# Kernel optimization log

Measured on AMD Instinct MI355X. Metric: run time of the kernel, lower is better.

## Reference

```python
import jax, jax.numpy as jnp
import numpy as np
from jax import lax

B, H, W, C = 4, 96, 96, 256
F = 256
KH = KW = 3
K = KH * KW
DG = 1
CG = C // DG
SH = SW = 1
DH = DW = 1
PAD_T = (DH * (KH - 1)) // 2  # 'same' padding (top/left) for 3x3 dil 1
PAD_L = (DW * (KW - 1)) // 2


def setup_inputs() -> dict:
    key = jax.random.key(0)
    k1, k2, k3 = jax.random.split(key, 3)
    x = jax.random.normal(k1, (B, H, W, C), jnp.float32)
    # offset/mask conv weights (orig init zeros; small random to exercise sampling)
    om_kernel = jax.random.normal(k2, (KH, KW, C, DG * 3 * K), jnp.float32) * 0.01
    om_bias = jnp.zeros((DG * 3 * K,), jnp.float32)
    stdv = 1.0 / np.sqrt(C * KH * KW)
    kernel = jax.random.uniform(k3, (K * C, F), jnp.float32, -stdv, stdv)
    bias = jnp.zeros((F,), jnp.float32)
    return {"x": x, "om_kernel": om_kernel, "om_bias": om_bias, "kernel": kernel, "bias": bias}


def reference(x, om_kernel, om_bias, kernel, bias):
    Bx, Hx, Wx, Cx = x.shape
    # offset/mask prediction conv (NHWC, 'SAME', matches keras Conv2D)
    om = lax.conv_general_dilated(
        x, om_kernel, (SH, SW), "SAME", rhs_dilation=(DH, DW),
        dimension_numbers=("NHWC", "HWIO", "NHWC")) + om_bias
    Ho, Wo = om.shape[1], om.shape[2]
    off = om[..., : 2 * DG * K].reshape(Bx, Ho, Wo, DG, K, 2)  # (dy, dx) per group/kpoint
    mask = jax.nn.sigmoid(om[..., 2 * DG * K :]).reshape(Bx, Ho, Wo, DG, K) * 2.0

    # base sampling grid: y = ho*SH - PAD_T + ki*DH (+ dy), similarly x
    base_y = (jnp.arange(Ho) * SH - PAD_T)[:, None] + (jnp.arange(KH) * DH)[None, :]  # [Ho,KH]
    base_x = (jnp.arange(Wo) * SW - PAD_L)[:, None] + (jnp.arange(KW) * DW)[None, :]  # [Wo,KW]
    gy = jnp.broadcast_to(base_y[:, None, :, None], (Ho, Wo, KH, KW)).reshape(Ho, Wo, K)
    gx = jnp.broadcast_to(base_x[None, :, None, :], (Ho, Wo, KH, KW)).reshape(Ho, Wo, K)

    py = gy[None, :, :, None, :].astype(x.dtype) + off[..., 0]  # [B,Ho,Wo,DG,K]
    px = gx[None, :, :, None, :].astype(x.dtype) + off[..., 1]

    # reorder to [B, N, DG] with N = Ho*Wo*K (K varies fastest after spatial)
    N = Ho * Wo * K
    py = py.transpose(0, 1, 2, 4, 3).reshape(Bx, N, DG)
    px = px.transpose(0, 1, 2, 4, 3).reshape(Bx, N, DG)
    mask_t = mask.transpose(0, 1, 2, 4, 3).reshape(Bx, N, DG)

    y0 = jnp.floor(py)
    x0 = jnp.floor(px)
    fy = py - y0
    fx = px - x0

    xf = x.reshape(Bx, Hx * Wx, DG, CG)
    val = jnp.zeros((Bx, N, DG, CG), x.dtype)
    for yi, wy in ((y0, 1.0 - fy), (y0 + 1.0, fy)):
        for xi, wx in ((x0, 1.0 - fx), (x0 + 1.0, fx)):
            valid = (yi >= 0) & (yi < Hx) & (xi >= 0) & (xi < Wx)
            yc = jnp.clip(yi, 0, Hx - 1).astype(jnp.int32)
            xc = jnp.clip(xi, 0, Wx - 1).astype(jnp.int32)
            lin = yc * Wx + xc  # [B,N,DG]
            g = jnp.take_along_axis(xf, lin[..., None], axis=1)  # [B,N,DG,CG]
            val = val + g * (wy * wx * valid.astype(x.dtype))[..., None]

    # modulate and im2col -> GEMM
    cols = (val * mask_t[..., None]).reshape(Bx, Ho * Wo, K * Cx)
    out = jnp.matmul(cols, kernel).reshape(Bx, Ho, Wo, -1) + bias
    return out
```

## Files before the change

kernel.cpp:

```cpp
#include <hip/hip_runtime.h>
#include <hip/hip_bf16.h>
#include <stdint.h>
#include <stddef.h>


namespace {
constexpr int H  = 96, W = 96, C = 256, F = 256;
constexpr int HP = 98;
constexpr int NP = 4 * 96 * 96;
constexpr int KC = 9 * 256;

constexpr int NB_PAD  = 4 * HP * HP / 8;
constexpr int NB_OMW  = 9 * 32;
constexpr int NB_WT   = (KC / 64) * (F / 64);
constexpr int NB_ZERO = NP * 32 * 4 / 4096;
}

typedef __attribute__((ext_vector_type(8))) short bf16x8;
typedef __attribute__((ext_vector_type(4))) float floatx4;

__device__ __forceinline__ void load_lds16(const void* g, void* l) {
  __builtin_amdgcn_global_load_lds((const __attribute__((address_space(1))) void*)g,
                                   (__attribute__((address_space(3))) void*)l,
                                   16, 0, 0);
}

__device__ __forceinline__ uint32_t pk2(float lo, float hi) {
  __hip_bfloat162 t = __float22bfloat162_rn(float2{lo, hi});
  return *reinterpret_cast<uint32_t*>(&t);
}

__device__ __forceinline__ void acc8(uint4 v, float w, float* a) {
  a[0] += w * __uint_as_float(v.x << 16); a[1] += w * __uint_as_float(v.x & 0xffff0000u);
  a[2] += w * __uint_as_float(v.y << 16); a[3] += w * __uint_as_float(v.y & 0xffff0000u);
  a[4] += w * __uint_as_float(v.z << 16); a[5] += w * __uint_as_float(v.z & 0xffff0000u);
  a[6] += w * __uint_as_float(v.w << 16); a[7] += w * __uint_as_float(v.w & 0xffff0000u);
}

__global__ __launch_bounds__(256) void k_prep(const float* __restrict__ x,
                                              const float* __restrict__ omk,
                                              const float* __restrict__ kern,
                                              uint4* __restrict__ xp4,
                                              __hip_bfloat16* __restrict__ wom,
                                              __hip_bfloat16* __restrict__ wt,
                                              float4* __restrict__ pOmz) {
  __shared__ float t[64][65];
  const int bi = blockIdx.x, tid = threadIdx.x;

  if (bi < NB_PAD) {
    const int sub = tid >> 5, cid = tid & 31;
    const int pp  = bi * 8 + sub;
    const int b   = pp / (HP * HP);
    const int r   = pp % (HP * HP);
    const int y   = r / HP, xq = r % HP;
    uint4 o = {0u, 0u, 0u, 0u};
    if (y >= 1 && y <= H && xq >= 1 && xq <= W) {
      const float* src = x + ((size_t)((b * H + (y - 1)) * W + (xq - 1))) * C + cid * 8;
      const float4 v0 = *(const float4*)src;
      const float4 v1 = *(const float4*)(src + 4);
      o.x = pk2(v0.x, v0.y); o.y = pk2(v0.z, v0.w);
      o.z = pk2(v1.x, v1.y); o.w = pk2(v1.z, v1.w);
    }
    xp4[(size_t)pp * 32 + cid] = o;
  } else if (bi < NB_PAD + NB_OMW) {
    const int i  = bi - NB_PAD;
    const int kk = i / 32, oc = i % 32;
    float v = (oc < 27) ? omk[(size_t)(kk * 256 + tid) * 27 + oc] : 0.f;
    wom[(size_t)oc * KC + kk * 256 + tid] = __float2bfloat16(v);
  } else if (bi < NB_PAD + NB_OMW + NB_WT) {
    const int j   = bi - NB_PAD - NB_OMW;
    const int kc0 = (j % (KC / 64)) * 64, f0 = (j / (KC / 64)) * 64;
    const int rr = tid >> 6, cc = tid & 63;
#pragma unroll
    for (int i = 0; i < 16; ++i)
      t[rr * 16 + i][cc] = kern[(size_t)(kc0 + rr * 16 + i) * F + f0 + cc];
    __syncthreads();
#pragma unroll
    for (int i = 0; i < 16; ++i) {
      const int frow = rr * 16 + i;
      wt[(size_t)(f0 + frow) * KC + kc0 + cc] = __float2bfloat16(t[cc][frow]);
    }
  } else {
    const int j = bi - NB_PAD - NB_OMW - NB_WT;
    pOmz[(size_t)j * 256 + tid] = (float4){0.f, 0.f, 0.f, 0.f};
  }
}

__global__ __launch_bounds__(256) void k_omgemm(const __hip_bfloat16* __restrict__ xp,
                                                const __hip_bfloat16* __restrict__ wom,
                                                float* __restrict__ pOm) {
  __shared__ __align__(16) char lds[10240];
  const int tid  = threadIdx.x;
  const int m0   = blockIdx.x * 128;
  const int s    = blockIdx.y;
  const int lane = tid & 63, wave = tid >> 6;
  const int quad = lane >> 4, l16 = lane & 15;

  const int kp = tid & 3;
  const __hip_bfloat16* abase[2];
#pragma unroll
  for (int j = 0; j < 2; ++j) {
    const int row = (tid >> 2) + j * 64;
    const int p = m0 + row;
    const int b = p / (H * W);
    const int hw = p % (H * W);
    const int h = hw / W, w = hw % W;
    abase[j] = xp + ((size_t)(b * HP + h) * HP + w) * C + kp * 8;
  }
  const __hip_bfloat16* bbase = wom + (size_t)(tid >> 2) * KC + kp * 8;

  floatx4 acc[2][2];
#pragma unroll
  for (int i = 0; i < 2; ++i)
#pragma unroll
    for (int j = 0; j < 2; ++j) acc[i][j] = (floatx4){0.f, 0.f, 0.f, 0.f};

  const int kbeg = s * 384;
#pragma unroll 1
  for (int k0 = kbeg; k0 < kbeg + 384; k0 += 32) {
    const int kk = k0 >> 8;
    const int c0 = k0 & 255;
    const int kh = kk / 3, kw = kk % 3;
    const int aoff = (kh * HP + kw) * C + c0;

    __syncthreads();
    load_lds16(abase[0] + aoff, &lds[tid * 16]);
    load_lds16(abase[1] + aoff, &lds[4096 + tid * 16]);
    if (tid < 128) load_lds16(bbase + k0, &lds[8192 + tid * 16]);
    __syncthreads();

    bf16x8 af[2], bfr[2];
#pragma unroll
    for (int mt = 0; mt < 2; ++mt)
      af[mt] = *(const bf16x8*)&lds[((wave * 32 + mt * 16 + l16) * 32 + quad * 8) * 2];
#pragma unroll
    for (int nt = 0; nt < 2; ++nt)
      bfr[nt] = *(const bf16x8*)&lds[8192 + ((nt * 16 + l16) * 32 + quad * 8) * 2];
#pragma unroll
    for (int mt = 0; mt < 2; ++mt)
#pragma unroll
      for (int nt = 0; nt < 2; ++nt)
        acc[mt][nt] = __builtin_amdgcn_mfma_f32_16x16x32_bf16(af[mt], bfr[nt], acc[mt][nt], 0, 0, 0);
  }

#pragma unroll
  for (int mt = 0; mt < 2; ++mt)
#pragma unroll
    for (int nt = 0; nt < 2; ++nt) {
      const int gm = m0 + wave * 32 + mt * 16 + quad * 4;
      const int gn = nt * 16 + l16;
#pragma unroll
      for (int r = 0; r < 4; ++r)
        __hip_atomic_fetch_add(&pOm[(size_t)(gm + r) * 32 + gn], acc[mt][nt][r],
                               __ATOMIC_RELAXED, __HIP_MEMORY_SCOPE_AGENT);
    }
}

__global__ __launch_bounds__(256) void k_sample(const uint4* __restrict__ xp4,
                                                const float* __restrict__ pOm,
                                                const float* __restrict__ om_bias,
                                                uint4* __restrict__ cols4) {
  __shared__ float2 s_ow[8][9][4];

  const int tid = threadIdx.x;
  const int sub = tid >> 5, cid = tid & 31;

  if (tid < 72) {
    const int ps = tid / 9, k = tid % 9;
    const int p  = blockIdx.x * 8 + ps;
    const int b  = p / (H * W);
    const int hw = p % (H * W);
    const int h = hw / W, w = hw % W;
    const float dy = om_bias[2 * k]     + pOm[(size_t)p * 32 + 2 * k];
    const float dx = om_bias[2 * k + 1] + pOm[(size_t)p * 32 + 2 * k + 1];
    const float mv = om_bias[18 + k]    + pOm[(size_t)p * 32 + 18 + k];
    const float m  = 2.f / (1.f + __expf(-mv));
    const float sy = (float)(h - 1 + k / 3) + dy;
    const float sx = (float)(w - 1 + k % 3) + dx;
    const float y0f = floorf(sy), x0f = floorf(sx);
    const float fy = sy - y0f, fx = sx - x0f;
    const int y0 = (int)y0f, x0 = (int)x0f;
#pragma unroll
    for (int c2 = 0; c2 < 4; ++c2) {
      const int dy2 = c2 >> 1, dx2 = c2 & 1;
      const int yi = y0 + dy2, xi = x0 + dx2;
      const bool valid = (yi >= 0) & (yi < H) & (xi >= 0) & (xi < W);
      const float wgt = valid ? (dy2 ? fy : 1.f - fy) * (dx2 ? fx : 1.f - fx) * m : 0.f;
      const int yc = min(max(yi + 1, 0), HP - 1);
      const int xc = min(max(xi + 1, 0), HP - 1);
      const int off = ((b * HP + yc) * HP + xc) * 32;
      s_ow[ps][k][c2] = float2{__int_as_float(off), wgt};
    }
  }
  __syncthreads();

  const int p = blockIdx.x * 8 + sub;
  uint4* __restrict__ ob = cols4 + (size_t)p * 288 + cid;

#pragma unroll 1
  for (int k = 0; k < 9; ++k) {
    const float2 ow0 = s_ow[sub][k][0], ow1 = s_ow[sub][k][1];
    const float2 ow2 = s_ow[sub][k][2], ow3 = s_ow[sub][k][3];
    float a[8] = {0.f, 0.f, 0.f, 0.f, 0.f, 0.f, 0.f, 0.f};
    acc8(xp4[(size_t)__float_as_int(ow0.x) + cid], ow0.y, a);
    acc8(xp4[(size_t)__float_as_int(ow1.x) + cid], ow1.y, a);
    acc8(xp4[(size_t)__float_as_int(ow2.x) + cid], ow2.y, a);
    acc8(xp4[(size_t)__float_as_int(ow3.x) + cid], ow3.y, a);
    uint4 o;
    o.x = pk2(a[0], a[1]); o.y = pk2(a[2], a[3]);
    o.z = pk2(a[4], a[5]); o.w = pk2(a[6], a[7]);
    ob[k * 32] = o;
  }
}

__global__ __launch_bounds__(256) void k_gemm(const __hip_bfloat16* __restrict__ A,
                                              const __hip_bfloat16* __restrict__ Bt,
                                              const float* __restrict__ bias,
                                              float* __restrict__ out) {
  __shared__ __align__(16) char lds[14336];

  const int tid  = threadIdx.x;
  const int m0   = blockIdx.x * 96;
  const int n0   = blockIdx.y * 128;
  const int lane = tid & 63, wave = tid >> 6;
  const int wm = wave & 1, wn = wave >> 1;
  const int quad = lane >> 4, l16 = lane & 15;

  floatx4 acc[3][4];
#pragma unroll
  for (int i = 0; i < 3; ++i)
#pragma unroll
    for (int j = 0; j < 4; ++j) acc[i][j] = (floatx4){0.f, 0.f, 0.f, 0.f};

#pragma unroll 1
  for (int k0 = 0; k0 < KC; k0 += 32) {
    __syncthreads();
    {
      const int row = tid >> 2, kp = tid & 3;
      load_lds16(A + (size_t)(m0 + row) * KC + k0 + kp * 8, &lds[tid * 16]);
      if (tid < 128)
        load_lds16(A + (size_t)(m0 + 64 + row) * KC + k0 + kp * 8, &lds[4096 + tid * 16]);
      load_lds16(Bt + (size_t)(n0 + row) * KC + k0 + kp * 8, &lds[6144 + tid * 16]);
      load_lds16(Bt + (size_t)(n0 + 64 + row) * KC + k0 + kp * 8, &lds[10240 + tid * 16]);
    }
    __syncthreads();

    bf16x8 af[3], bfr[4];
#pragma unroll
    for (int mt = 0; mt < 3; ++mt)
      af[mt] = *(const bf16x8*)&lds[((wm * 48 + mt * 16 + l16) * 32 + quad * 8) * 2];
#pragma unroll
    for (int nt = 0; nt < 4; ++nt)
      bfr[nt] = *(const bf16x8*)&lds[6144 + ((wn * 64 + nt * 16 + l16) * 32 + quad * 8) * 2];
#pragma unroll
    for (int mt = 0; mt < 3; ++mt)
#pragma unroll
      for (int nt = 0; nt < 4; ++nt)
        acc[mt][nt] = __builtin_amdgcn_mfma_f32_16x16x32_bf16(af[mt], bfr[nt], acc[mt][nt], 0, 0, 0);
  }

#pragma unroll
  for (int mt = 0; mt < 3; ++mt) {
#pragma unroll
    for (int nt = 0; nt < 4; ++nt) {
      const int gm = m0 + wm * 48 + mt * 16 + quad * 4;
      const int gn = n0 + wn * 64 + nt * 16 + l16;
      const float bs = bias[gn];
#pragma unroll
      for (int r = 0; r < 4; ++r)
        out[(size_t)(gm + r) * F + gn] = acc[mt][nt][r] + bs;
    }
  }
}

extern "C" void kernel_launch(void* const* d_in, const int* in_sizes, int n_in,
                              void* d_out, int out_size, void* d_ws, size_t ws_size,
                              hipStream_t stream) {
  const float* x    = (const float*)d_in[0];
  const float* omk  = (const float*)d_in[1];
  const float* omb  = (const float*)d_in[2];
  const float* kern = (const float*)d_in[3];
  const float* bias = (const float*)d_in[4];
  float* out = (float*)d_out;

  char* ws = (char*)d_ws;
  size_t off = 0;
  __hip_bfloat16* wt   = (__hip_bfloat16*)(ws + off); off += (size_t)F * KC * 2;
  __hip_bfloat16* xp   = (__hip_bfloat16*)(ws + off); off += (size_t)4 * HP * HP * C * 2;
  __hip_bfloat16* wom  = (__hip_bfloat16*)(ws + off); off += (size_t)32 * KC * 2;
  float*          pOm  = (float*)(ws + off);          off += (size_t)NP * 32 * 4;
  __hip_bfloat16* cols = (__hip_bfloat16*)(ws + off);

  k_prep  <<<dim3(NB_PAD + NB_OMW + NB_WT + NB_ZERO), 256, 0, stream>>>(
      x, omk, kern, (uint4*)xp, wom, wt, (float4*)pOm);
  k_omgemm<<<dim3(NP / 128, 6),      256, 0, stream>>>(xp, wom, pOm);
  k_sample<<<dim3(NP / 8),           256, 0, stream>>>((const uint4*)xp, pOm, omb, (uint4*)cols);
  k_gemm  <<<dim3(NP / 96, F / 128), 256, 0, stream>>>(cols, wt, bias, out);
}
```

Baseline: 227.5 us.

## Fuse deformable bilinear sampling into the main GEMM, dropping the cols buffer

Merges the sampling kernel and the main GEMM into one kernel. Each block builds a 48-row A tile in LDS directly from bilinear samples of the padded input, instead of writing a large bf16 im2col buffer to global memory and reading it back. The block covers the full N=256 with a swizzled B tile, uses a K step of 64, and remaps block indices across the grid. In exchange, gather latency now sits on the GEMM critical path without overlap, B is reloaded by every block, and occupancy drops because of higher LDS use.

```diff
diff --git a/kernel.cpp b/kernel.cpp
--- a/kernel.cpp
+++ b/kernel.cpp
@@ -156,24 +156,33 @@
     }
 }
 
-__global__ __launch_bounds__(256) void k_sample(const uint4* __restrict__ xp4,
-                                                const float* __restrict__ pOm,
-                                                const float* __restrict__ om_bias,
-                                                uint4* __restrict__ cols4) {
-  __shared__ float2 s_ow[8][9][4];
-
-  const int tid = threadIdx.x;
-  const int sub = tid >> 5, cid = tid & 31;
-
-  if (tid < 72) {
-    const int ps = tid / 9, k = tid % 9;
-    const int p  = blockIdx.x * 8 + ps;
+__global__ __launch_bounds__(256, 3) void k_fused(const uint4* __restrict__ xpu,
+                                                  const float* __restrict__ pOm,
+                                                  const float* __restrict__ omb,
+                                                  const __hip_bfloat16* __restrict__ Bt,
+                                                  const float* __restrict__ bias,
+                                                  float* __restrict__ out) {
+  __shared__ __align__(16) char  s_a[48 * 144];
+  __shared__ __align__(16) char  s_b[32768];
+  __shared__ float2 s_ow[48 * 9 * 4];
+
+  const int tid  = threadIdx.x;
+  const int bx   = blockIdx.x;
+  const int lt   = (bx & 7) * 96 + (bx >> 3);
+  const int m0   = lt * 48;
+  const int lane = tid & 63, wave = tid >> 6;
+  const int quad = lane >> 4, l16 = lane & 15;
+
+#pragma unroll 1
+  for (int i = tid; i < 48 * 9; i += 256) {
+    const int ps = i % 48, k = i / 48;
+    const int p  = m0 + ps;
     const int b  = p / (H * W);
     const int hw = p % (H * W);
     const int h = hw / W, w = hw % W;
-    const float dy = om_bias[2 * k]     + pOm[(size_t)p * 32 + 2 * k];
-    const float dx = om_bias[2 * k + 1] + pOm[(size_t)p * 32 + 2 * k + 1];
-    const float mv = om_bias[18 + k]    + pOm[(size_t)p * 32 + 18 + k];
+    const float dy = omb[2 * k]     + pOm[(size_t)p * 32 + 2 * k];
+    const float dx = omb[2 * k + 1] + pOm[(size_t)p * 32 + 2 * k + 1];
+    const float mv = omb[18 + k]    + pOm[(size_t)p * 32 + 18 + k];
     const float m  = 2.f / (1.f + __expf(-mv));
     const float sy = (float)(h - 1 + k / 3) + dy;
     const float sx = (float)(w - 1 + k % 3) + dx;
@@ -189,82 +198,86 @@
       const int yc = min(max(yi + 1, 0), HP - 1);
       const int xc = min(max(xi + 1, 0), HP - 1);
       const int off = ((b * HP + yc) * HP + xc) * 32;
-      s_ow[ps][k][c2] = float2{__int_as_float(off), wgt};
-    }
-  }
-  __syncthreads();
-
-  const int p = blockIdx.x * 8 + sub;
-  uint4* __restrict__ ob = cols4 + (size_t)p * 288 + cid;
+      s_ow[(ps * 9 + k) * 4 + c2] = float2{__int_as_float(off), wgt};
+    }
+  }
+
+  floatx4 acc[3][4];
+#pragma unroll
+  for (int i = 0; i < 3; ++i)
+#pragma unroll
+    for (int j = 0; j < 4; ++j) acc[i][j] = (floatx4){0.f, 0.f, 0.f, 0.f};
+
+  const int ps = tid >> 2, grp = tid & 3;
 
 #pragma unroll 1
-  for (int k = 0; k < 9; ++k) {
-    const float2 ow0 = s_ow[sub][k][0], ow1 = s_ow[sub][k][1];
-    const float2 ow2 = s_ow[sub][k][2], ow3 = s_ow[sub][k][3];
-    float a[8] = {0.f, 0.f, 0.f, 0.f, 0.f, 0.f, 0.f, 0.f};
-    acc8(xp4[(size_t)__float_as_int(ow0.x) + cid], ow0.y, a);
-    acc8(xp4[(size_t)__float_as_int(ow1.x) + cid], ow1.y, a);
-    acc8(xp4[(size_t)__float_as_int(ow2.x) + cid], ow2.y, a);
-    acc8(xp4[(size_t)__float_as_int(ow3.x) + cid], ow3.y, a);
-    uint4 o;
-    o.x = pk2(a[0], a[1]); o.y = pk2(a[2], a[3]);
-    o.z = pk2(a[4], a[5]); o.w = pk2(a[6], a[7]);
-    ob[k * 32] = o;
-  }
-}
-
-__global__ __launch_bounds__(256) void k_gemm(const __hip_bfloat16* __restrict__ A,
-                                              const __hip_bfloat16* __restrict__ Bt,
-                                              const float* __restrict__ bias,
-                                              float* __restrict__ out) {
-  __shared__ __align__(16) char lds[14336];
-
-  const int tid  = threadIdx.x;
-  const int m0   = blockIdx.x * 96;
-  const int n0   = blockIdx.y * 128;
-  const int lane = tid & 63, wave = tid >> 6;
-  const int wm = wave & 1, wn = wave >> 1;
-  const int quad = lane >> 4, l16 = lane & 15;
-
-  floatx4 acc[3][4];
-#pragma unroll
-  for (int i = 0; i < 3; ++i)
-#pragma unroll
-    for (int j = 0; j < 4; ++j) acc[i][j] = (floatx4){0.f, 0.f, 0.f, 0.f};
-
-#pragma unroll 1
-  for (int k0 = 0; k0 < KC; k0 += 32) {
-    __syncthreads();
-    {
-      const int row = tid >> 2, kp = tid & 3;
-      load_lds16(A + (size_t)(m0 + row) * KC + k0 + kp * 8, &lds[tid * 16]);
-      if (tid < 128)
-        load_lds16(A + (size_t)(m0 + 64 + row) * KC + k0 + kp * 8, &lds[4096 + tid * 16]);
-      load_lds16(Bt + (size_t)(n0 + row) * KC + k0 + kp * 8, &lds[6144 + tid * 16]);
-      load_lds16(Bt + (size_t)(n0 + 64 + row) * KC + k0 + kp * 8, &lds[10240 + tid * 16]);
-    }
-    __syncthreads();
-
-    bf16x8 af[3], bfr[4];
+  for (int k0 = 0; k0 < KC; k0 += 64) {
+    const int kk = k0 >> 8;
+    const int cb = (k0 & 255) >> 3;
+
+    __syncthreads();
+#pragma unroll
+    for (int j = 0; j < 8; ++j) {
+      const int g = tid + j * 256;
+      const int c = g >> 8, rp = g & 255;
+      const int n = (rp - 2 * c) & 255;
+      load_lds16(Bt + (size_t)n * KC + k0 + c * 8, &s_b[g * 16]);
+    }
+    if (tid < 192) {
+      const float2* owp = &s_ow[(ps * 9 + kk) * 4];
+      float a[16];
+#pragma unroll
+      for (int t = 0; t < 16; ++t) a[t] = 0.f;
+#pragma unroll
+      for (int c2 = 0; c2 < 4; ++c2) {
+        const float2 ow = owp[c2];
+        const uint4* src = xpu + (size_t)__float_as_int(ow.x) + cb + grp * 2;
+        const uint4 v0 = src[0], v1 = src[1];
+        acc8(v0, ow.y, a);
+        acc8(v1, ow.y, a + 8);
+      }
+      uint4 o0, o1;
+      o0.x = pk2(a[0], a[1]);   o0.y = pk2(a[2], a[3]);
+      o0.z = pk2(a[4], a[5]);   o0.w = pk2(a[6], a[7]);
+      o1.x = pk2(a[8], a[9]);   o1.y = pk2(a[10], a[11]);
+      o1.z = pk2(a[12], a[13]); o1.w = pk2(a[14], a[15]);
+      char* dst = &s_a[ps * 144 + grp * 32];
+      *(uint4*)dst = o0;
+      *(uint4*)(dst + 16) = o1;
+    }
+    __syncthreads();
+
+    bf16x8 af[3][2], bfr[4][2];
 #pragma unroll
     for (int mt = 0; mt < 3; ++mt)
-      af[mt] = *(const bf16x8*)&lds[((wm * 48 + mt * 16 + l16) * 32 + quad * 8) * 2];
+#pragma unroll
+      for (int c = 0; c < 2; ++c)
+        af[mt][c] = *(const bf16x8*)&s_a[(mt * 16 + l16) * 144 + c * 64 + quad * 16];
 #pragma unroll
     for (int nt = 0; nt < 4; ++nt)
-      bfr[nt] = *(const bf16x8*)&lds[6144 + ((wn * 64 + nt * 16 + l16) * 32 + quad * 8) * 2];
-#pragma unroll
-    for (int mt = 0; mt < 3; ++mt)
-#pragma unroll
-      for (int nt = 0; nt < 4; ++nt)
-        acc[mt][nt] = __builtin_amdgcn_mfma_f32_16x16x32_bf16(af[mt], bfr[nt], acc[mt][nt], 0, 0, 0);
+#pragma unroll
+      for (int c = 0; c < 2; ++c) {
+        const int cc   = c * 4 + quad;
+        const int n    = wave * 64 + nt * 16 + l16;
+        const int slot = cc * 256 + ((n + 2 * cc) & 255);
+        bfr[nt][c] = *(const bf16x8*)&s_b[slot * 16];
+      }
+#pragma unroll
+    for (int c = 0; c < 2; ++c)
+#pragma unroll
+      for (int mt = 0; mt < 3; ++mt)
+#pragma unroll
+        for (int nt = 0; nt < 4; ++nt)
+          acc[mt][nt] = __builtin_amdgcn_mfma_f32_16x16x32_bf16(af[mt][c], bfr[nt][c],
+                                                                acc[mt][nt], 0, 0, 0);
   }
 
 #pragma unroll
   for (int mt = 0; mt < 3; ++mt) {
 #pragma unroll
     for (int nt = 0; nt < 4; ++nt) {
-      const int gm = m0 + wm * 48 + mt * 16 + quad * 4;
-      const int gn = n0 + wn * 64 + nt * 16 + l16;
+      const int gm = m0 + mt * 16 + quad * 4;
+      const int gn = wave * 64 + nt * 16 + l16;
       const float bs = bias[gn];
 #pragma unroll
       for (int r = 0; r < 4; ++r)
@@ -289,11 +302,9 @@
   __hip_bfloat16* xp   = (__hip_bfloat16*)(ws + off); off += (size_t)4 * HP * HP * C * 2;
   __hip_bfloat16* wom  = (__hip_bfloat16*)(ws + off); off += (size_t)32 * KC * 2;
   float*          pOm  = (float*)(ws + off);          off += (size_t)NP * 32 * 4;
-  __hip_bfloat16* cols = (__hip_bfloat16*)(ws + off);
 
   k_prep  <<<dim3(NB_PAD + NB_OMW + NB_WT + NB_ZERO), 256, 0, stream>>>(
       x, omk, kern, (uint4*)xp, wom, wt, (float4*)pOm);
-  k_omgemm<<<dim3(NP / 128, 6),      256, 0, stream>>>(xp, wom, pOm);
-  k_sample<<<dim3(NP / 8),           256, 0, stream>>>((const uint4*)xp, pOm, omb, (uint4*)cols);
-  k_gemm  <<<dim3(NP / 96, F / 128), 256, 0, stream>>>(cols, wt, bias, out);
-}
+  k_omgemm<<<dim3(NP / 128, 6), 256, 0, stream>>>(xp, wom, pOm);
+  k_fused <<<dim3(NP / 48),     256, 0, stream>>>((const uint4*)xp, pOm, omb, wt, bias, out);
+}
```

Result: slower. 298.9 us (+31.4%).
